# Optimization experiments

Measured on AMD Instinct MI355X. Metric: run time of the kernel, lower is better.

## Reference

```python
import jax, jax.numpy as jnp
import numpy as np

B = 512        # number of graphs
NPG = 128      # nodes per graph
N = B * NPG    # total nodes = 65536
E = 262144     # total edges (intra-graph)
F_IN = 128     # input features
H = 256        # hidden
C = 2          # num classes
BN_EPS = 1e-5


def _lin_params(key, fan_in, fan_out):
    k1, k2 = jax.random.split(key)
    s = 1.0 / np.sqrt(fan_in)
    w = jax.random.uniform(k1, (fan_in, fan_out), jnp.float32, -s, s)
    b = jax.random.uniform(k2, (fan_out,), jnp.float32, -s, s)
    return w, b


def setup_inputs() -> dict:
    key = jax.random.key(0)
    ks = jax.random.split(key, 16)
    x = jax.random.normal(ks[0], (N, F_IN), jnp.float32)
    # intra-graph random edges (required for assignment pooling semantics)
    rng = np.random.RandomState(0)
    g = np.repeat(np.arange(B), E // B)
    src = g * NPG + rng.randint(0, NPG, E)
    dst = g * NPG + rng.randint(0, NPG, E)
    edge_index = jnp.asarray(np.stack([src, dst]), jnp.int64 if jax.config.jax_enable_x64 else jnp.int32)
    batch = jnp.repeat(jnp.arange(B), NPG)
    # GIN layer 0 (F_IN->H->H) + BN
    w0_1, b0_1 = _lin_params(ks[1], F_IN, H)
    w0_2, b0_2 = _lin_params(ks[2], H, H)
    g0 = jnp.ones((H,), jnp.float32); be0 = jnp.zeros((H,), jnp.float32)
    # GIN layers 1..2 stacked (H->H->H) + BN
    wl1 = jnp.stack([_lin_params(jax.random.fold_in(ks[3], i), H, H)[0] for i in range(2)])
    bl1 = jnp.stack([_lin_params(jax.random.fold_in(ks[3], i), H, H)[1] for i in range(2)])
    wl2 = jnp.stack([_lin_params(jax.random.fold_in(ks[4], i), H, H)[0] for i in range(2)])
    bl2 = jnp.stack([_lin_params(jax.random.fold_in(ks[4], i), H, H)[1] for i in range(2)])
    gl = jnp.ones((2, H), jnp.float32); bel = jnp.zeros((2, H), jnp.float32)
    c1w, c1b = _lin_params(ks[5], H, H)
    c2w, c2b = _lin_params(ks[6], H, 2)
    l1w, l1b = _lin_params(ks[7], H, H)
    l2w, l2b = _lin_params(ks[8], H, C)
    return dict(x=x, edge_index=edge_index, batch=batch,
                w0_1=w0_1, b0_1=b0_1, w0_2=w0_2, b0_2=b0_2, g0=g0, be0=be0,
                wl1=wl1, bl1=bl1, wl2=wl2, bl2=bl2, gl=gl, bel=bel,
                c1w=c1w, c1b=c1b, c2w=c2w, c2b=c2b,
                l1w=l1w, l1b=l1b, l2w=l2w, l2b=l2b)


def _gin_layer(h, src, dst, w1, b1, w2, b2, gamma, beta):
    # GINConv (eps=0): MLP(h + sum_{j in N(i)} h_j)
    agg = jax.ops.segment_sum(h[src], dst, num_segments=N)
    z = h + agg
    z = jax.nn.relu(z @ w1 + b1)
    z = jax.nn.relu(z @ w2 + b2)
    # BatchNorm1d, training-mode batch stats (biased variance)
    mu = jnp.mean(z, axis=0)
    var = jnp.mean((z - mu) ** 2, axis=0)
    return (z - mu) * jax.lax.rsqrt(var + BN_EPS) * gamma + beta


def reference(x, edge_index, batch, w0_1, b0_1, w0_2, b0_2, g0, be0,
              wl1, bl1, wl2, bl2, gl, bel,
              c1w, c1b, c2w, c2b, l1w, l1b, l2w, l2b):
    src, dst = edge_index[0], edge_index[1]
    h = _gin_layer(x, src, dst, w0_1, b0_1, w0_2, b0_2, g0, be0)
    for i in range(2):
        h = _gin_layer(h, src, dst, wl1[i], bl1[i], wl2[i], bl2[i], gl[i], bel[i])
    # assignment: softmax(cluster2(tanh(cluster1(h))))  -> [N, 2]
    a = jax.nn.softmax(jnp.tanh(h @ c1w + c1b) @ c2w + c2b, axis=1)
    # subgraph embedding: (assignment^T @ x)[0] per graph == segment-sum of a[:,0]*h
    sub = jax.ops.segment_sum(a[:, :1] * h, batch, num_segments=B)        # [B, H]
    # graph embedding: per-graph mean of h
    cnt = jax.ops.segment_sum(jnp.ones((N,), h.dtype), batch, num_segments=B)
    graph = jax.ops.segment_sum(h, batch, num_segments=B) / cnt[:, None]   # [B, H]
    # new_adj[g] = A_g^T-pooled: sum over edges outer(a[src], a[dst]) -> [B,2,2]
    new_adj = jax.ops.segment_sum(a[src][:, :, None] * a[dst][:, None, :], batch[src], num_segments=B)
    # F.normalize(p=1, dim=1) row-wise, then diagonal, MSE vs ones(2)
    rown = jnp.maximum(jnp.sum(jnp.abs(new_adj), axis=2, keepdims=True), 1e-12)
    norm_adj = new_adj / rown
    diag = jnp.diagonal(norm_adj, axis1=1, axis2=2)                        # [B, 2]
    con_penalty = jnp.mean(jnp.mean((diag - 1.0) ** 2, axis=1))
    # classifier head (dropout in eval mode -> identity)
    z = jax.nn.relu(sub @ l1w + l1b)
    out = jax.nn.log_softmax(z @ l2w + l2b, axis=-1)
    return out, sub, graph, con_penalty
```

## Files before the change

### kernel.cpp

```cpp
#include <hip/hip_runtime.h>
#include <stdint.h>

#define NN 65536
#define NB 512
#define NPG 128
#define NE 262144
#define EPG 512
#define HD 256
#define BN_EPS 1e-5f

typedef unsigned short u16;
typedef float f32x4 __attribute__((ext_vector_type(4)));
typedef __bf16 bf16x8 __attribute__((ext_vector_type(8)));
typedef unsigned short u16x8 __attribute__((ext_vector_type(8)));
typedef unsigned short u16x4 __attribute__((ext_vector_type(4)));

__device__ __forceinline__ float b2f(u16 u){
  union { unsigned i; float f; } x; x.i = ((unsigned)u) << 16; return x.f;
}
__device__ __forceinline__ u16 f2b(float f){
  union { float f; unsigned i; } x; x.f = f;
  unsigned r = x.i + 0x7fffu + ((x.i >> 16) & 1u);
  return (u16)(r >> 16);
}
__device__ __forceinline__ float ftanh(float x){
  float e = __expf(2.0f * x);
  return 1.0f - 2.0f * __builtin_amdgcn_rcpf(e + 1.0f);
}
__device__ __forceinline__ bf16x8 u8x8_to_bf16x8(unsigned d0, unsigned d1){
  u16x8 r;
  #pragma unroll
  for (int b = 0; b < 4; b++){
    union { float f; unsigned u; } x, y;
    x.f = (float)((d0 >> (b * 8)) & 255u);
    y.f = (float)((d1 >> (b * 8)) & 255u);
    r[b] = (u16)(x.u >> 16);
    r[4 + b] = (u16)(y.u >> 16);
  }
  return *(bf16x8*)&r;
}

__global__ void __launch_bounds__(256) pack_all(
    const float* __restrict__ w0_1, const float* __restrict__ w0_2,
    const float* __restrict__ wl1, const float* __restrict__ wl2,
    const float* __restrict__ c1w,
    u16* i01, u16* i02, u16* il1a, u16* il1b, u16* il2a, u16* il2b, u16* ic1)
{
  const int seg = blockIdx.y;
  const int idx = blockIdx.x * 256 + threadIdx.x;
  const float* W; u16* img; int K = 256;
  switch (seg){
    case 0: W = w0_1;        img = i01;  K = 128; break;
    case 1: W = w0_2;        img = i02;  break;
    case 2: W = wl1;         img = il1a; break;
    case 3: W = wl1 + 65536; img = il1b; break;
    case 4: W = wl2;         img = il2a; break;
    case 5: W = wl2 + 65536; img = il2b; break;
    default: W = c1w;        img = ic1;  break;
  }
  if (idx >= K * 256) return;
  int col = idx / K, k = idx - col * K;
  img[idx] = f2b(W[(size_t)k * 256 + col]);
}

template<int KIN, int MODE>
__global__ void __launch_bounds__(512, 2) layer_kernel(
    const void* __restrict__ hin_, const int* __restrict__ ei,
    const float* __restrict__ sc, const float* __restrict__ sh,
    const u16* __restrict__ w1img, const float* __restrict__ b1,
    const u16* __restrict__ w2img, const float* __restrict__ b2,
    u16* __restrict__ Y, float* __restrict__ pS, float* __restrict__ pQ)
{
  __shared__ __align__(16) char smem[KIN * 256 + 65536 + 16384];
  char* ht  = smem;
  char* g1t = smem + KIN * 256;
  unsigned* A32 = (unsigned*)(smem + KIN * 256 + 65536);
  char* Ab = (char*)A32;

  const int g = blockIdx.x, tid = threadIdx.x;
  const int lane = tid & 63, wid = tid >> 6;
  const int l15 = lane & 15, lk = (lane >> 4) * 8;
  const int c0 = wid * 32;

  #pragma unroll
  for (int i = 0; i < 8; i++) A32[tid + i * 512] = 0u;
  __syncthreads();

  {
    int s = ei[g * EPG + tid] & (NPG - 1);
    int d = ei[NE + g * EPG + tid] & (NPG - 1);
    unsigned byte = ((unsigned)((d << 7) | (s & ~3))) ^ ((unsigned)((d & 7) << 4));
    atomicAdd(&A32[byte >> 2], 1u << ((s & 3) * 8));
  }
  if (tid < NPG){
    int n = tid;
    unsigned byte = ((unsigned)((n << 7) | (n & ~3))) ^ ((unsigned)((n & 7) << 4));
    atomicAdd(&A32[byte >> 2], 1u << ((n & 3) * 8));
  }

  if constexpr (MODE == 0){
    const float* hin = (const float*)hin_;
    #pragma unroll
    for (int i = 0; i < 4; i++){
      int idx = tid + i * 512;
      int row = idx >> 4, c8 = idx & 15;
      const float* p = hin + (size_t)(g * NPG + row) * KIN + c8 * 8;
      float4 v0 = *(const float4*)p;
      float4 v1 = *(const float4*)(p + 4);
      u16x8 o;
      o[0] = f2b(v0.x); o[1] = f2b(v0.y); o[2] = f2b(v0.z); o[3] = f2b(v0.w);
      o[4] = f2b(v1.x); o[5] = f2b(v1.y); o[6] = f2b(v1.z); o[7] = f2b(v1.w);
      unsigned byte = ((unsigned)(row * (KIN * 2) + c8 * 16)) ^ ((unsigned)((row & 7) << 4));
      *(u16x8*)(ht + byte) = o;
    }
  } else {
    const u16* hin = (const u16*)hin_;
    const int c8 = tid & 31;
    float scr[8], shr[8];
    {
      float4 a0 = *(const float4*)(sc + c8 * 8);
      float4 a1 = *(const float4*)(sc + c8 * 8 + 4);
      float4 s0 = *(const float4*)(sh + c8 * 8);
      float4 s1 = *(const float4*)(sh + c8 * 8 + 4);
      scr[0]=a0.x; scr[1]=a0.y; scr[2]=a0.z; scr[3]=a0.w;
      scr[4]=a1.x; scr[5]=a1.y; scr[6]=a1.z; scr[7]=a1.w;
      shr[0]=s0.x; shr[1]=s0.y; shr[2]=s0.z; shr[3]=s0.w;
      shr[4]=s1.x; shr[5]=s1.y; shr[6]=s1.z; shr[7]=s1.w;
    }
    #pragma unroll
    for (int i = 0; i < 8; i++){
      int idx = tid + i * 512;
      int row = idx >> 5;
      u16x8 v = *(const u16x8*)(hin + (size_t)(g * NPG + row) * KIN + c8 * 8);
      u16x8 o;
      #pragma unroll
      for (int k = 0; k < 8; k++) o[k] = f2b(b2f(v[k]) * scr[k] + shr[k]);
      unsigned byte = ((unsigned)(row * (KIN * 2) + c8 * 16)) ^ ((unsigned)((row & 7) << 4));
      *(u16x8*)(ht + byte) = o;
    }
  }
  __syncthreads();

  {
    f32x4 acc[8][2] = {};
    #pragma unroll
    for (int kk = 0; kk < KIN / 32; kk++){
      bf16x8 bfr[2];
      #pragma unroll
      for (int nf = 0; nf < 2; nf++)
        bfr[nf] = *(const bf16x8*)(w1img + (size_t)(c0 + nf * 16 + l15) * KIN + kk * 32 + lk);
      bf16x8 af[8];
      #pragma unroll
      for (int mf = 0; mf < 8; mf++){
        int row = mf * 16 + l15;
        unsigned byte = ((unsigned)(row * (KIN * 2) + (kk * 32 + lk) * 2)) ^ ((unsigned)((row & 7) << 4));
        af[mf] = *(const bf16x8*)(ht + byte);
      }
      #pragma unroll
      for (int mf = 0; mf < 8; mf++)
        #pragma unroll
        for (int nf = 0; nf < 2; nf++)
          acc[mf][nf] = __builtin_amdgcn_mfma_f32_16x16x32_bf16(af[mf], bfr[nf], acc[mf][nf], 0, 0, 0);
    }
    #pragma unroll
    for (int mf = 0; mf < 8; mf++)
      #pragma unroll
      for (int nf = 0; nf < 2; nf++){
        int c = c0 + nf * 16 + l15;
        int n0 = mf * 16 + (lane >> 4) * 4;
        u16x4 o;
        #pragma unroll
        for (int j = 0; j < 4; j++) o[j] = f2b(acc[mf][nf][j]);
        unsigned byte = ((unsigned)(c * 256 + n0 * 2)) ^ ((unsigned)((c & 7) << 4));
        *(u16x4*)(g1t + byte) = o;
      }
  }

  {
    f32x4 acc[8][2] = {};
    bf16x8 gfr[4][2];
    #pragma unroll
    for (int kk = 0; kk < 4; kk++)
      #pragma unroll
      for (int cf = 0; cf < 2; cf++){
        int c = c0 + cf * 16 + l15;
        unsigned byte = ((unsigned)(c * 256 + (kk * 32 + lk) * 2)) ^ ((unsigned)((c & 7) << 4));
        gfr[kk][cf] = *(const bf16x8*)(g1t + byte);
      }
    #pragma unroll
    for (int kk = 0; kk < 4; kk++){
      bf16x8 bfA[8];
      #pragma unroll
      for (int nf = 0; nf < 8; nf++){
        int n = nf * 16 + l15;
        unsigned byte = ((unsigned)((n << 7) + kk * 32 + lk)) ^ ((unsigned)((n & 7) << 4));
        uint2 dd = *(const uint2*)(Ab + byte);
        bfA[nf] = u8x8_to_bf16x8(dd.x, dd.y);
      }
      #pragma unroll
      for (int nf = 0; nf < 8; nf++)
        #pragma unroll
        for (int cf = 0; cf < 2; cf++)
          acc[nf][cf] = __builtin_amdgcn_mfma_f32_16x16x32_bf16(gfr[kk][cf], bfA[nf], acc[nf][cf], 0, 0, 0);
    }
    __syncthreads();
    #pragma unroll
    for (int nf = 0; nf < 8; nf++)
      #pragma unroll
      for (int cf = 0; cf < 2; cf++){
        int n = nf * 16 + l15;
        int cb = c0 + cf * 16 + (lane >> 4) * 4;
        float4 bv = *(const float4*)(b1 + cb);
        u16x4 o;
        o[0] = f2b(fmaxf(acc[nf][cf][0] + bv.x, 0.f));
        o[1] = f2b(fmaxf(acc[nf][cf][1] + bv.y, 0.f));
        o[2] = f2b(fmaxf(acc[nf][cf][2] + bv.z, 0.f));
        o[3] = f2b(fmaxf(acc[nf][cf][3] + bv.w, 0.f));
        unsigned byte = ((unsigned)(n * 512 + cb * 2)) ^ ((unsigned)((n & 7) << 4));
        *(u16x4*)(g1t + byte) = o;
      }
  }
  __syncthreads();

  {
    f32x4 acc[8][2] = {};
    #pragma unroll
    for (int kk = 0; kk < 8; kk++){
      bf16x8 bfr[2];
      #pragma unroll
      for (int cf = 0; cf < 2; cf++)
        bfr[cf] = *(const bf16x8*)(w2img + (size_t)(c0 + cf * 16 + l15) * 256 + kk * 32 + lk);
      bf16x8 zf[8];
      #pragma unroll
      for (int nf = 0; nf < 8; nf++){
        int n = nf * 16 + l15;
        unsigned byte = ((unsigned)(n * 512 + (kk * 32 + lk) * 2)) ^ ((unsigned)((n & 7) << 4));
        zf[nf] = *(const bf16x8*)(g1t + byte);
      }
      #pragma unroll
      for (int nf = 0; nf < 8; nf++)
        #pragma unroll
        for (int cf = 0; cf < 2; cf++)
          acc[nf][cf] = __builtin_amdgcn_mfma_f32_16x16x32_bf16(bfr[cf], zf[nf], acc[nf][cf], 0, 0, 0);
    }
    float sv[2][4] = {}, qv[2][4] = {};
    #pragma unroll
    for (int nf = 0; nf < 8; nf++)
      #pragma unroll
      for (int cf = 0; cf < 2; cf++){
        int n = nf * 16 + l15;
        int cb = c0 + cf * 16 + (lane >> 4) * 4;
        float4 bv = *(const float4*)(b2 + cb);
        u16x4 o;
        float v0 = fmaxf(acc[nf][cf][0] + bv.x, 0.f);
        float v1 = fmaxf(acc[nf][cf][1] + bv.y, 0.f);
        float v2 = fmaxf(acc[nf][cf][2] + bv.z, 0.f);
        float v3 = fmaxf(acc[nf][cf][3] + bv.w, 0.f);
        o[0] = f2b(v0); o[1] = f2b(v1); o[2] = f2b(v2); o[3] = f2b(v3);
        sv[cf][0] += v0; sv[cf][1] += v1; sv[cf][2] += v2; sv[cf][3] += v3;
        qv[cf][0] += v0 * v0; qv[cf][1] += v1 * v1; qv[cf][2] += v2 * v2; qv[cf][3] += v3 * v3;
        *(u16x4*)(Y + (size_t)(g * NPG + n) * HD + cb) = o;
      }
    #pragma unroll
    for (int m = 1; m <= 8; m <<= 1)
      #pragma unroll
      for (int cf = 0; cf < 2; cf++)
        #pragma unroll
        for (int j = 0; j < 4; j++){
          sv[cf][j] += __shfl_xor(sv[cf][j], m);
          qv[cf][j] += __shfl_xor(qv[cf][j], m);
        }
    if (l15 == 0){
      int jb = (lane >> 4) * 4;
      #pragma unroll
      for (int cf = 0; cf < 2; cf++)
        #pragma unroll
        for (int j = 0; j < 4; j++){
          int col = c0 + cf * 16 + jb + j;
          pS[(size_t)col * NB + g] = sv[cf][j];
          pQ[(size_t)col * NB + g] = qv[cf][j];
        }
    }
  }
}

__global__ void __launch_bounds__(64) bnfin_kernel(const float* __restrict__ pS,
    const float* __restrict__ pQ, const float* __restrict__ gma,
    const float* __restrict__ bta, float* __restrict__ scale, float* __restrict__ shift)
{
  int c = blockIdx.x, lane = threadIdx.x;
  float s = 0.f, q = 0.f;
  for (int i = lane; i < NB; i += 64){ s += pS[(size_t)c * NB + i]; q += pQ[(size_t)c * NB + i]; }
  for (int m = 32; m; m >>= 1){ s += __shfl_xor(s, m); q += __shfl_xor(q, m); }
  if (lane == 0){
    float mu = s * (1.0f / NN);
    float var = q * (1.0f / NN) - mu * mu;
    float scv = gma[c] * rsqrtf(var + BN_EPS);
    scale[c] = scv;
    shift[c] = bta[c] - mu * scv;
  }
}

template<int K>
__device__ __forceinline__ void mm_frag(const u16* Alds,
    const u16* __restrict__ wimg, int lane, int c0, f32x4 (&acc)[8][2])
{
  const int l15 = lane & 15, lk = (lane >> 4) * 8;
  bf16x8 bfr[K / 32][2];
  #pragma unroll
  for (int kk = 0; kk < K / 32; kk++)
    #pragma unroll
    for (int nf = 0; nf < 2; nf++)
      bfr[kk][nf] = *(const bf16x8*)(wimg + (size_t)(c0 + nf * 16 + l15) * K + kk * 32 + lk);
  #pragma unroll
  for (int kk = 0; kk < K / 32; kk++){
    bf16x8 af[8];
    #pragma unroll
    for (int mf = 0; mf < 8; mf++){
      int row = mf * 16 + l15;
      unsigned byte = ((unsigned)(row * (K * 2) + (kk * 32 + lk) * 2)) ^ (unsigned)((row & 7) << 4);
      af[mf] = *(const bf16x8*)((const char*)Alds + byte);
    }
    #pragma unroll
    for (int mf = 0; mf < 8; mf++)
      #pragma unroll
      for (int nf = 0; nf < 2; nf++)
        acc[mf][nf] = __builtin_amdgcn_mfma_f32_16x16x32_bf16(af[mf], bfr[kk][nf], acc[mf][nf], 0, 0, 0);
  }
}

__global__ void __launch_bounds__(512) final_kernel(
    const u16* __restrict__ hin, const int* __restrict__ ei,
    const float* __restrict__ sc, const float* __restrict__ sh,
    const u16* __restrict__ c1img, const float* __restrict__ c1b,
    const float* __restrict__ c2w, const float* __restrict__ c2b,
    const float* __restrict__ l1w, const float* __restrict__ l1b,
    const float* __restrict__ l2w, const float* __restrict__ l2b,
    float* __restrict__ outLog, float* __restrict__ outSub,
    float* __restrict__ outGraph, float* __restrict__ outPen)
{
  __shared__ u16 ht[NPG * HD];
  __shared__ u16 esd[EPG];
  __shared__ float aL[NPG * 2];
  __shared__ float scratch[2048];
  __shared__ float subL[256];
  __shared__ float wred[8][4];
  const int g = blockIdx.x, tid = threadIdx.x;
  const int lane = tid & 63, wid = tid >> 6;

  if (tid < 256){ scratch[tid] = sc[tid]; scratch[256 + tid] = sh[tid]; }
  {
    int s = ei[g * EPG + tid] & (NPG - 1);
    int d = ei[NE + g * EPG + tid] & (NPG - 1);
    esd[tid] = (u16)(s | (d << 8));
  }
  __syncthreads();

  #pragma unroll
  for (int i = 0; i < 8; i++){
    int idx = tid + i * 512;
    int row = idx >> 5, c8 = idx & 31;
    u16x8 v = *(const u16x8*)(hin + (size_t)(g * NPG + row) * HD + c8 * 8);
    u16x8 o;
    #pragma unroll
    for (int k = 0; k < 8; k++)
      o[k] = f2b(b2f(v[k]) * scratch[c8 * 8 + k] + scratch[256 + c8 * 8 + k]);
    unsigned byte = ((unsigned)(row * 512 + c8 * 16)) ^ (unsigned)((row & 7) << 4);
    *(u16x8*)((char*)ht + byte) = o;
  }
  __syncthreads();

  const int c0 = wid * 32;
  const int l15 = lane & 15;

  {
    f32x4 acct[8][2] = {};
    mm_frag<HD>(ht, c1img, lane, c0, acct);
    const int col0 = c0 + l15, col1 = c0 + 16 + l15;
    const float bv0 = c1b[col0], bv1 = c1b[col1];
    const float w00 = c2w[col0 * 2], w01 = c2w[col0 * 2 + 1];
    const float w10 = c2w[col1 * 2], w11 = c2w[col1 * 2 + 1];
    #pragma unroll
    for (int mf = 0; mf < 8; mf++)
      #pragma unroll
      for (int j = 0; j < 4; j++){
        float t0 = ftanh(acct[mf][0][j] + bv0);
        float t1 = ftanh(acct[mf][1][j] + bv1);
        float p0 = t0 * w00 + t1 * w10;
        float p1 = t0 * w01 + t1 * w11;
        p0 += __shfl_xor(p0, 1); p0 += __shfl_xor(p0, 2);
        p0 += __shfl_xor(p0, 4); p0 += __shfl_xor(p0, 8);
        p1 += __shfl_xor(p1, 1); p1 += __shfl_xor(p1, 2);
        p1 += __shfl_xor(p1, 4); p1 += __shfl_xor(p1, 8);
        if (l15 == 0){
          int row = mf * 16 + (lane >> 4) * 4 + j;
          scratch[row * 16 + wid * 2]     = p0;
          scratch[row * 16 + wid * 2 + 1] = p1;
        }
      }
  }
  __syncthreads();

  {
    int row = tid >> 2, part = tid & 3;
    float4 v = *(const float4*)&scratch[row * 16 + part * 4];
    float p0 = v.x + v.z, p1 = v.y + v.w;
    p0 += __shfl_xor(p0, 1); p0 += __shfl_xor(p0, 2);
    p1 += __shfl_xor(p1, 1); p1 += __shfl_xor(p1, 2);
    if (part == 0){
      p0 += c2b[0]; p1 += c2b[1];
      float mx = fmaxf(p0, p1);
      float e0 = expf(p0 - mx), e1 = expf(p1 - mx);
      float inv = 1.f / (e0 + e1);
      aL[row * 2] = e0 * inv; aL[row * 2 + 1] = e1 * inv;
    }
  }
  __syncthreads();

  {
    int v = esd[tid];
    int sE = v & 255, dE = v >> 8;
    float as0 = aL[sE * 2], as1 = aL[sE * 2 + 1];
    float ad0 = aL[dE * 2], ad1 = aL[dE * 2 + 1];
    float m00 = as0 * ad0, m01 = as0 * ad1, m10 = as1 * ad0, m11 = as1 * ad1;
    #pragma unroll
    for (int m = 1; m < 64; m <<= 1){
      m00 += __shfl_xor(m00, m); m01 += __shfl_xor(m01, m);
      m10 += __shfl_xor(m10, m); m11 += __shfl_xor(m11, m);
    }
    if (lane == 0){ wred[wid][0] = m00; wred[wid][1] = m01; wred[wid][2] = m10; wred[wid][3] = m11; }
  }
  {
    const int part = tid >> 8, c = tid & 255;
    float sb = 0.f, gs = 0.f;
    #pragma unroll 8
    for (int i = 0; i < 64; i++){
      int n = part * 64 + i;
      unsigned byte = ((unsigned)(n * 512 + c * 2)) ^ (unsigned)((n & 7) << 4);
      float v = b2f(*(const u16*)((const char*)ht + byte));
      sb += aL[n * 2] * v; gs += v;
    }
    __syncthreads();
    scratch[part * 512 + c] = sb;
    scratch[part * 512 + 256 + c] = gs;
  }
  __syncthreads();
  if (tid < 256){
    float sb = scratch[tid] + scratch[512 + tid];
    float gs = scratch[256 + tid] + scratch[768 + tid];
    subL[tid] = sb;
    outSub[(size_t)g * HD + tid] = sb;
    outGraph[(size_t)g * HD + tid] = gs * (1.f / NPG);
  }
  if (tid == 0){
    float m00 = 0, m01 = 0, m10 = 0, m11 = 0;
    for (int w = 0; w < 8; w++){ m00 += wred[w][0]; m01 += wred[w][1]; m10 += wred[w][2]; m11 += wred[w][3]; }
    float r0 = fmaxf(fabsf(m00) + fabsf(m01), 1e-12f);
    float r1 = fmaxf(fabsf(m10) + fabsf(m11), 1e-12f);
    float d0 = m00 / r0 - 1.f, d1 = m11 / r1 - 1.f;
    atomicAdd(outPen, 0.5f * (d0 * d0 + d1 * d1) * (1.0f / NB));
  }
  __syncthreads();

  {
    const int ph = tid >> 8, c = tid & 255;
    float z = 0.f;
    for (int k = ph * 128; k < ph * 128 + 128; k++)
      z += subL[k] * l1w[(size_t)k * HD + c];
    scratch[ph * 256 + c] = z;
  }
  __syncthreads();
  if (tid < 256){
    float z = fmaxf(scratch[tid] + scratch[256 + tid] + l1b[tid], 0.f);
    float o0 = z * l2w[tid * 2], o1 = z * l2w[tid * 2 + 1];
    #pragma unroll
    for (int m = 1; m < 64; m <<= 1){ o0 += __shfl_xor(o0, m); o1 += __shfl_xor(o1, m); }
    if (lane == 0){ wred[wid][0] = o0; wred[wid][1] = o1; }
  }
  __syncthreads();
  if (tid == 0){
    float o0 = wred[0][0] + wred[1][0] + wred[2][0] + wred[3][0] + l2b[0];
    float o1 = wred[0][1] + wred[1][1] + wred[2][1] + wred[3][1] + l2b[1];
    float mx = fmaxf(o0, o1);
    float lse = mx + logf(expf(o0 - mx) + expf(o1 - mx));
    outLog[(size_t)g * 2] = o0 - lse;
    outLog[(size_t)g * 2 + 1] = o1 - lse;
  }
}

extern "C" void kernel_launch(void* const* d_in, const int* in_sizes, int n_in,
                              void* d_out, int out_size, void* d_ws, size_t ws_size,
                              hipStream_t stream)
{
  (void)in_sizes; (void)n_in; (void)out_size; (void)ws_size;
  const float* x    = (const float*)d_in[0];
  const int*   ei   = (const int*)  d_in[1];
  const float* w0_1 = (const float*)d_in[3];
  const float* b0_1 = (const float*)d_in[4];
  const float* w0_2 = (const float*)d_in[5];
  const float* b0_2 = (const float*)d_in[6];
  const float* g0   = (const float*)d_in[7];
  const float* be0  = (const float*)d_in[8];
  const float* wl1  = (const float*)d_in[9];
  const float* bl1  = (const float*)d_in[10];
  const float* wl2  = (const float*)d_in[11];
  const float* bl2  = (const float*)d_in[12];
  const float* gl   = (const float*)d_in[13];
  const float* bel  = (const float*)d_in[14];
  const float* c1w  = (const float*)d_in[15];
  const float* c1b  = (const float*)d_in[16];
  const float* c2w  = (const float*)d_in[17];
  const float* c2b  = (const float*)d_in[18];
  const float* l1w  = (const float*)d_in[19];
  const float* l1b  = (const float*)d_in[20];
  const float* l2w  = (const float*)d_in[21];
  const float* l2b  = (const float*)d_in[22];
  float* out = (float*)d_out;

  char* cur = (char*)d_ws;
  auto carve = [&](size_t bytes) -> void* {
    void* p = (void*)cur; cur += (bytes + 255) & ~(size_t)255; return p;
  };
  u16* B0    = (u16*)carve((size_t)NN * HD * 2);
  u16* B1    = (u16*)carve((size_t)NN * HD * 2);
  u16* i01   = (u16*)carve((size_t)128 * 256 * 2);
  u16* i02   = (u16*)carve((size_t)256 * 256 * 2);
  u16* il1a  = (u16*)carve((size_t)256 * 256 * 2);
  u16* il1b  = (u16*)carve((size_t)256 * 256 * 2);
  u16* il2a  = (u16*)carve((size_t)256 * 256 * 2);
  u16* il2b  = (u16*)carve((size_t)256 * 256 * 2);
  u16* ic1   = (u16*)carve((size_t)256 * 256 * 2);
  float* pS  = (float*)carve((size_t)256 * NB * 4);
  float* pQ  = (float*)carve((size_t)256 * NB * 4);
  float* bsc = (float*)carve(256 * 4);
  float* bsh = (float*)carve(256 * 4);

  float* outPen = out + 1024 + 2 * NB * HD;

  pack_all<<<dim3(256, 7), 256, 0, stream>>>(w0_1, w0_2, wl1, wl2, c1w,
                                             i01, i02, il1a, il1b, il2a, il2b, ic1);
  hipMemsetAsync((void*)outPen, 0, 4, stream);

  layer_kernel<128, 0><<<NB, 512, 0, stream>>>((const void*)x, ei, nullptr, nullptr,
                                               i01, b0_1, i02, b0_2, B0, pS, pQ);
  bnfin_kernel<<<256, 64, 0, stream>>>(pS, pQ, g0, be0, bsc, bsh);

  layer_kernel<256, 1><<<NB, 512, 0, stream>>>((const void*)B0, ei, bsc, bsh,
                                               il1a, bl1, il2a, bl2, B1, pS, pQ);
  bnfin_kernel<<<256, 64, 0, stream>>>(pS, pQ, gl, bel, bsc, bsh);

  layer_kernel<256, 1><<<NB, 512, 0, stream>>>((const void*)B1, ei, bsc, bsh,
                                               il1b, bl1 + 256, il2b, bl2 + 256, B0, pS, pQ);
  bnfin_kernel<<<256, 64, 0, stream>>>(pS, pQ, gl + 256, bel + 256, bsc, bsh);

  final_kernel<<<NB, 512, 0, stream>>>(B0, ei, bsc, bsh, ic1, c1b, c2w, c2b,
                                       l1w, l1b, l2w, l2b,
                                       out, out + 1024, out + 1024 + NB * HD, outPen);
}
```

Baseline: 293.4 us.

## Fold BN finalize into consumer kernels and alias LDS buffers for higher occupancy

Removes the three separate bnfin_kernel launches. Each consumer block now reduces the per-graph partial sums itself, with the partials stored graph-major so those reads are contiguous across threads. The layer kernel's input tile and intermediate tile now share one 64KB LDS region, with an added barrier between the first GEMM and the intermediate writes. Launch bounds are raised to 4 blocks per CU. The trade is that every block redundantly reads 2×512×256 floats of partials (about 1MB per block from L2), and the higher launch bound may force register spills given the large accumulator arrays.

```diff
diff --git a/kernel.cpp b/kernel.cpp
--- a/kernel.cpp
+++ b/kernel.cpp
@@ -64,17 +64,17 @@
 }
 
 template<int KIN, int MODE>
-__global__ void __launch_bounds__(512, 2) layer_kernel(
+__global__ void __launch_bounds__(512, 4) layer_kernel(
     const void* __restrict__ hin_, const int* __restrict__ ei,
-    const float* __restrict__ sc, const float* __restrict__ sh,
+    const float* __restrict__ pSin, const float* __restrict__ pQin,
+    const float* __restrict__ gma, const float* __restrict__ bta,
     const u16* __restrict__ w1img, const float* __restrict__ b1,
     const u16* __restrict__ w2img, const float* __restrict__ b2,
     u16* __restrict__ Y, float* __restrict__ pS, float* __restrict__ pQ)
 {
-  __shared__ __align__(16) char smem[KIN * 256 + 65536 + 16384];
-  char* ht  = smem;
-  char* g1t = smem + KIN * 256;
-  unsigned* A32 = (unsigned*)(smem + KIN * 256 + 65536);
+  __shared__ __align__(16) char smem[65536 + 16384];
+  char* act = smem;
+  unsigned* A32 = (unsigned*)(smem + 65536);
   char* Ab = (char*)A32;
 
   const int g = blockIdx.x, tid = threadIdx.x;
@@ -84,6 +84,30 @@
 
   #pragma unroll
   for (int i = 0; i < 8; i++) A32[tid + i * 512] = 0u;
+
+  float scr[8], shr[8];
+  if constexpr (MODE == 1){
+    float scv = 0.f, shv = 0.f;
+    if (tid < 256){
+      float s = 0.f, q = 0.f;
+      #pragma unroll 8
+      for (int i = 0; i < NB; i++){
+        s += pSin[(size_t)i * 256 + tid];
+        q += pQin[(size_t)i * 256 + tid];
+      }
+      float mu = s * (1.0f / NN);
+      float var = q * (1.0f / NN) - mu * mu;
+      scv = gma[tid] * rsqrtf(var + BN_EPS);
+      shv = bta[tid] - mu * scv;
+    }
+    __syncthreads();
+    float* ldsf = (float*)act;
+    if (tid < 256){ ldsf[tid] = scv; ldsf[256 + tid] = shv; }
+    __syncthreads();
+    const int c8 = tid & 31;
+    #pragma unroll
+    for (int k = 0; k < 8; k++){ scr[k] = ldsf[c8 * 8 + k]; shr[k] = ldsf[256 + c8 * 8 + k]; }
+  }
   __syncthreads();
 
   {
@@ -111,22 +135,11 @@
       o[0] = f2b(v0.x); o[1] = f2b(v0.y); o[2] = f2b(v0.z); o[3] = f2b(v0.w);
       o[4] = f2b(v1.x); o[5] = f2b(v1.y); o[6] = f2b(v1.z); o[7] = f2b(v1.w);
       unsigned byte = ((unsigned)(row * (KIN * 2) + c8 * 16)) ^ ((unsigned)((row & 7) << 4));
-      *(u16x8*)(ht + byte) = o;
+      *(u16x8*)(act + byte) = o;
     }
   } else {
     const u16* hin = (const u16*)hin_;
     const int c8 = tid & 31;
-    float scr[8], shr[8];
-    {
-      float4 a0 = *(const float4*)(sc + c8 * 8);
-      float4 a1 = *(const float4*)(sc + c8 * 8 + 4);
-      float4 s0 = *(const float4*)(sh + c8 * 8);
-      float4 s1 = *(const float4*)(sh + c8 * 8 + 4);
-      scr[0]=a0.x; scr[1]=a0.y; scr[2]=a0.z; scr[3]=a0.w;
-      scr[4]=a1.x; scr[5]=a1.y; scr[6]=a1.z; scr[7]=a1.w;
-      shr[0]=s0.x; shr[1]=s0.y; shr[2]=s0.z; shr[3]=s0.w;
-      shr[4]=s1.x; shr[5]=s1.y; shr[6]=s1.z; shr[7]=s1.w;
-    }
     #pragma unroll
     for (int i = 0; i < 8; i++){
       int idx = tid + i * 512;
@@ -136,13 +149,13 @@
       #pragma unroll
       for (int k = 0; k < 8; k++) o[k] = f2b(b2f(v[k]) * scr[k] + shr[k]);
       unsigned byte = ((unsigned)(row * (KIN * 2) + c8 * 16)) ^ ((unsigned)((row & 7) << 4));
-      *(u16x8*)(ht + byte) = o;
-    }
-  }
-  __syncthreads();
-
-  {
-    f32x4 acc[8][2] = {};
+      *(u16x8*)(act + byte) = o;
+    }
+  }
+  __syncthreads();
+
+  f32x4 acc[8][2] = {};
+  {
     #pragma unroll
     for (int kk = 0; kk < KIN / 32; kk++){
       bf16x8 bfr[2];
@@ -154,7 +167,7 @@
       for (int mf = 0; mf < 8; mf++){
         int row = mf * 16 + l15;
         unsigned byte = ((unsigned)(row * (KIN * 2) + (kk * 32 + lk) * 2)) ^ ((unsigned)((row & 7) << 4));
-        af[mf] = *(const bf16x8*)(ht + byte);
+        af[mf] = *(const bf16x8*)(act + byte);
       }
       #pragma unroll
       for (int mf = 0; mf < 8; mf++)
@@ -162,22 +175,24 @@
         for (int nf = 0; nf < 2; nf++)
           acc[mf][nf] = __builtin_amdgcn_mfma_f32_16x16x32_bf16(af[mf], bfr[nf], acc[mf][nf], 0, 0, 0);
     }
-    #pragma unroll
-    for (int mf = 0; mf < 8; mf++)
-      #pragma unroll
-      for (int nf = 0; nf < 2; nf++){
-        int c = c0 + nf * 16 + l15;
-        int n0 = mf * 16 + (lane >> 4) * 4;
-        u16x4 o;
-        #pragma unroll
-        for (int j = 0; j < 4; j++) o[j] = f2b(acc[mf][nf][j]);
-        unsigned byte = ((unsigned)(c * 256 + n0 * 2)) ^ ((unsigned)((c & 7) << 4));
-        *(u16x4*)(g1t + byte) = o;
-      }
-  }
-
-  {
-    f32x4 acc[8][2] = {};
+  }
+  __syncthreads();
+
+  #pragma unroll
+  for (int mf = 0; mf < 8; mf++)
+    #pragma unroll
+    for (int nf = 0; nf < 2; nf++){
+      int c = c0 + nf * 16 + l15;
+      int n0 = mf * 16 + (lane >> 4) * 4;
+      u16x4 o;
+      #pragma unroll
+      for (int j = 0; j < 4; j++) o[j] = f2b(acc[mf][nf][j]);
+      unsigned byte = ((unsigned)(c * 256 + n0 * 2)) ^ ((unsigned)((c & 7) << 4));
+      *(u16x4*)(act + byte) = o;
+    }
+
+  {
+    f32x4 acc2[8][2] = {};
     bf16x8 gfr[4][2];
     #pragma unroll
     for (int kk = 0; kk < 4; kk++)
@@ -185,7 +200,7 @@
       for (int cf = 0; cf < 2; cf++){
         int c = c0 + cf * 16 + l15;
         unsigned byte = ((unsigned)(c * 256 + (kk * 32 + lk) * 2)) ^ ((unsigned)((c & 7) << 4));
-        gfr[kk][cf] = *(const bf16x8*)(g1t + byte);
+        gfr[kk][cf] = *(const bf16x8*)(act + byte);
       }
     #pragma unroll
     for (int kk = 0; kk < 4; kk++){
@@ -201,7 +216,7 @@
       for (int nf = 0; nf < 8; nf++)
         #pragma unroll
         for (int cf = 0; cf < 2; cf++)
-          acc[nf][cf] = __builtin_amdgcn_mfma_f32_16x16x32_bf16(gfr[kk][cf], bfA[nf], acc[nf][cf], 0, 0, 0);
+          acc2[nf][cf] = __builtin_amdgcn_mfma_f32_16x16x32_bf16(gfr[kk][cf], bfA[nf], acc2[nf][cf], 0, 0, 0);
     }
     __syncthreads();
     #pragma unroll
@@ -212,18 +227,18 @@
         int cb = c0 + cf * 16 + (lane >> 4) * 4;
         float4 bv = *(const float4*)(b1 + cb);
         u16x4 o;
-        o[0] = f2b(fmaxf(acc[nf][cf][0] + bv.x, 0.f));
-        o[1] = f2b(fmaxf(acc[nf][cf][1] + bv.y, 0.f));
-        o[2] = f2b(fmaxf(acc[nf][cf][2] + bv.z, 0.f));
-        o[3] = f2b(fmaxf(acc[nf][cf][3] + bv.w, 0.f));
+        o[0] = f2b(fmaxf(acc2[nf][cf][0] + bv.x, 0.f));
+        o[1] = f2b(fmaxf(acc2[nf][cf][1] + bv.y, 0.f));
+        o[2] = f2b(fmaxf(acc2[nf][cf][2] + bv.z, 0.f));
+        o[3] = f2b(fmaxf(acc2[nf][cf][3] + bv.w, 0.f));
         unsigned byte = ((unsigned)(n * 512 + cb * 2)) ^ ((unsigned)((n & 7) << 4));
-        *(u16x4*)(g1t + byte) = o;
-      }
-  }
-  __syncthreads();
-
-  {
-    f32x4 acc[8][2] = {};
+        *(u16x4*)(act + byte) = o;
+      }
+  }
+  __syncthreads();
+
+  {
+    f32x4 acc3[8][2] = {};
     #pragma unroll
     for (int kk = 0; kk < 8; kk++){
       bf16x8 bfr[2];
@@ -235,13 +250,13 @@
       for (int nf = 0; nf < 8; nf++){
         int n = nf * 16 + l15;
         unsigned byte = ((unsigned)(n * 512 + (kk * 32 + lk) * 2)) ^ ((unsigned)((n & 7) << 4));
-        zf[nf] = *(const bf16x8*)(g1t + byte);
+        zf[nf] = *(const bf16x8*)(act + byte);
       }
       #pragma unroll
       for (int nf = 0; nf < 8; nf++)
         #pragma unroll
         for (int cf = 0; cf < 2; cf++)
-          acc[nf][cf] = __builtin_amdgcn_mfma_f32_16x16x32_bf16(bfr[cf], zf[nf], acc[nf][cf], 0, 0, 0);
+          acc3[nf][cf] = __builtin_amdgcn_mfma_f32_16x16x32_bf16(bfr[cf], zf[nf], acc3[nf][cf], 0, 0, 0);
     }
     float sv[2][4] = {}, qv[2][4] = {};
     #pragma unroll
@@ -252,10 +267,10 @@
         int cb = c0 + cf * 16 + (lane >> 4) * 4;
         float4 bv = *(const float4*)(b2 + cb);
         u16x4 o;
-        float v0 = fmaxf(acc[nf][cf][0] + bv.x, 0.f);
-        float v1 = fmaxf(acc[nf][cf][1] + bv.y, 0.f);
-        float v2 = fmaxf(acc[nf][cf][2] + bv.z, 0.f);
-        float v3 = fmaxf(acc[nf][cf][3] + bv.w, 0.f);
+        float v0 = fmaxf(acc3[nf][cf][0] + bv.x, 0.f);
+        float v1 = fmaxf(acc3[nf][cf][1] + bv.y, 0.f);
+        float v2 = fmaxf(acc3[nf][cf][2] + bv.z, 0.f);
+        float v3 = fmaxf(acc3[nf][cf][3] + bv.w, 0.f);
         o[0] = f2b(v0); o[1] = f2b(v1); o[2] = f2b(v2); o[3] = f2b(v3);
         sv[cf][0] += v0; sv[cf][1] += v1; sv[cf][2] += v2; sv[cf][3] += v3;
         qv[cf][0] += v0 * v0; qv[cf][1] += v1 * v1; qv[cf][2] += v2 * v2; qv[cf][3] += v3 * v3;
@@ -277,27 +292,10 @@
         #pragma unroll
         for (int j = 0; j < 4; j++){
           int col = c0 + cf * 16 + jb + j;
-          pS[(size_t)col * NB + g] = sv[cf][j];
-          pQ[(size_t)col * NB + g] = qv[cf][j];
+          pS[(size_t)g * 256 + col] = sv[cf][j];
+          pQ[(size_t)g * 256 + col] = qv[cf][j];
         }
     }
-  }
-}
-
-__global__ void __launch_bounds__(64) bnfin_kernel(const float* __restrict__ pS,
-    const float* __restrict__ pQ, const float* __restrict__ gma,
-    const float* __restrict__ bta, float* __restrict__ scale, float* __restrict__ shift)
-{
-  int c = blockIdx.x, lane = threadIdx.x;
-  float s = 0.f, q = 0.f;
-  for (int i = lane; i < NB; i += 64){ s += pS[(size_t)c * NB + i]; q += pQ[(size_t)c * NB + i]; }
-  for (int m = 32; m; m >>= 1){ s += __shfl_xor(s, m); q += __shfl_xor(q, m); }
-  if (lane == 0){
-    float mu = s * (1.0f / NN);
-    float var = q * (1.0f / NN) - mu * mu;
-    float scv = gma[c] * rsqrtf(var + BN_EPS);
-    scale[c] = scv;
-    shift[c] = bta[c] - mu * scv;
   }
 }
 
@@ -331,7 +329,8 @@
 
 __global__ void __launch_bounds__(512) final_kernel(
     const u16* __restrict__ hin, const int* __restrict__ ei,
-    const float* __restrict__ sc, const float* __restrict__ sh,
+    const float* __restrict__ pSin, const float* __restrict__ pQin,
+    const float* __restrict__ gma, const float* __restrict__ bta,
     const u16* __restrict__ c1img, const float* __restrict__ c1b,
     const float* __restrict__ c2w, const float* __restrict__ c2b,
     const float* __restrict__ l1w, const float* __restrict__ l1b,
@@ -348,7 +347,19 @@
   const int g = blockIdx.x, tid = threadIdx.x;
   const int lane = tid & 63, wid = tid >> 6;
 
-  if (tid < 256){ scratch[tid] = sc[tid]; scratch[256 + tid] = sh[tid]; }
+  if (tid < 256){
+    float s = 0.f, q = 0.f;
+    #pragma unroll 8
+    for (int i = 0; i < NB; i++){
+      s += pSin[(size_t)i * 256 + tid];
+      q += pQin[(size_t)i * 256 + tid];
+    }
+    float mu = s * (1.0f / NN);
+    float var = q * (1.0f / NN) - mu * mu;
+    float scv = gma[tid] * rsqrtf(var + BN_EPS);
+    scratch[tid] = scv;
+    scratch[256 + tid] = bta[tid] - mu * scv;
+  }
   {
     int s = ei[g * EPG + tid] & (NPG - 1);
     int d = ei[NE + g * EPG + tid] & (NPG - 1);
@@ -530,10 +541,12 @@
   u16* il2a  = (u16*)carve((size_t)256 * 256 * 2);
   u16* il2b  = (u16*)carve((size_t)256 * 256 * 2);
   u16* ic1   = (u16*)carve((size_t)256 * 256 * 2);
-  float* pS  = (float*)carve((size_t)256 * NB * 4);
-  float* pQ  = (float*)carve((size_t)256 * NB * 4);
-  float* bsc = (float*)carve(256 * 4);
-  float* bsh = (float*)carve(256 * 4);
+  float* pS0 = (float*)carve((size_t)NB * 256 * 4);
+  float* pQ0 = (float*)carve((size_t)NB * 256 * 4);
+  float* pS1 = (float*)carve((size_t)NB * 256 * 4);
+  float* pQ1 = (float*)carve((size_t)NB * 256 * 4);
+  float* pS2 = (float*)carve((size_t)NB * 256 * 4);
+  float* pQ2 = (float*)carve((size_t)NB * 256 * 4);
 
   float* outPen = out + 1024 + 2 * NB * HD;
 
@@ -541,19 +554,16 @@
                                              i01, i02, il1a, il1b, il2a, il2b, ic1);
   hipMemsetAsync((void*)outPen, 0, 4, stream);
 
-  layer_kernel<128, 0><<<NB, 512, 0, stream>>>((const void*)x, ei, nullptr, nullptr,
-                                               i01, b0_1, i02, b0_2, B0, pS, pQ);
-  bnfin_kernel<<<256, 64, 0, stream>>>(pS, pQ, g0, be0, bsc, bsh);
-
-  layer_kernel<256, 1><<<NB, 512, 0, stream>>>((const void*)B0, ei, bsc, bsh,
-                                               il1a, bl1, il2a, bl2, B1, pS, pQ);
-  bnfin_kernel<<<256, 64, 0, stream>>>(pS, pQ, gl, bel, bsc, bsh);
-
-  layer_kernel<256, 1><<<NB, 512, 0, stream>>>((const void*)B1, ei, bsc, bsh,
-                                               il1b, bl1 + 256, il2b, bl2 + 256, B0, pS, pQ);
-  bnfin_kernel<<<256, 64, 0, stream>>>(pS, pQ, gl + 256, bel + 256, bsc, bsh);
-
-  final_kernel<<<NB, 512, 0, stream>>>(B0, ei, bsc, bsh, ic1, c1b, c2w, c2b,
-                                       l1w, l1b, l2w, l2b,
+  layer_kernel<128, 0><<<NB, 512, 0, stream>>>((const void*)x, ei,
+      nullptr, nullptr, nullptr, nullptr, i01, b0_1, i02, b0_2, B0, pS0, pQ0);
+
+  layer_kernel<256, 1><<<NB, 512, 0, stream>>>((const void*)B0, ei,
+      pS0, pQ0, g0, be0, il1a, bl1, il2a, bl2, B1, pS1, pQ1);
+
+  layer_kernel<256, 1><<<NB, 512, 0, stream>>>((const void*)B1, ei,
+      pS1, pQ1, gl, bel, il1b, bl1 + 256, il2b, bl2 + 256, B0, pS2, pQ2);
+
+  final_kernel<<<NB, 512, 0, stream>>>(B0, ei, pS2, pQ2, gl + 256, bel + 256,
+                                       ic1, c1b, c2w, c2b, l1w, l1b, l2w, l2b,
                                        out, out + 1024, out + 1024 + NB * HD, outPen);
 }
```

Result: slower. 362.9 us (+23.7%).
